# Kernel tuning notes

Hardware: AMD Instinct MI355X
Metric: run time of the kernel (lower is better)

## Reference

```python
import jax, jax.numpy as jnp
import numpy as np

H = 0.1  # explicit-Euler step size

def double_layer(x, K1, K2):
    # 1x1 conv1d == channel matmul; conv -> tanh -> conv
    x = jnp.tanh(jnp.einsum('oc,bcn->bon', K1, x))
    return jnp.einsum('oc,bcn->bon', K2, x)

def setup_inputs() -> dict:
    key = jax.random.key(0)
    ks = jax.random.split(key, 14)
    B, nNin, nEin, nopen, nhid, nNclose, nlayer = 1, 64, 64, 128, 128, 64, 4
    N, E = 10000, 160000
    Nfeat = 3 * nopen  # varlet=False
    stdv, stdvp = 0.01, 0.001
    return {
        'xn': jax.random.normal(ks[0], (B, nNin, N), dtype=jnp.float32),
        'xe': jax.random.normal(ks[1], (B, nEin, E), dtype=jnp.float32),
        'iInd': jax.random.randint(ks[2], (E,), 0, N),
        'jInd': jax.random.randint(ks[3], (E,), 0, N),
        'nnodes': N,
        'K1Nopen': jax.random.normal(ks[4], (nopen, nNin)) * stdv,
        'K2Nopen': jax.random.normal(ks[5], (nopen, nopen)) * stdv,
        'K1Eopen': jax.random.normal(ks[6], (nopen, nEin)) * stdv,
        'K2Eopen': jax.random.normal(ks[7], (nopen, nopen)) * stdv,
        'KNclose': jax.random.normal(ks[8], (nNclose, nopen)) * stdv,
        'KE1': jax.random.normal(ks[9], (nlayer, nhid, Nfeat)) * stdvp,
        'KE2': jax.random.normal(ks[10], (nlayer, nopen, nhid)) * stdvp,
        'KN1': jax.random.normal(ks[11], (nlayer, nhid, Nfeat)) * stdvp,
        'KN2': jax.random.normal(ks[12], (nlayer, nopen, nhid)) * stdvp,
    }

def reference(xn, xe, iInd, jInd, nnodes, K1Nopen, K2Nopen, K1Eopen, K2Eopen,
              KNclose, KE1, KE2, KN1, KN2):
    xn = double_layer(xn, K1Nopen, K2Nopen)   # [B, nopen, N]
    xe = double_layer(xe, K1Eopen, K2Eopen)   # [B, nopen, E]
    nlayer = KE1.shape[0]
    for i in range(nlayer):
        xi = xn[:, :, iInd]
        xj = xn[:, :, jInd]
        gradX = xi - xj                        # Graph.nodeGrad
        intX = 0.5 * (xi + xj)                 # Graph.nodeAve
        dxe = jnp.concatenate([intX, xe, gradX], axis=1)  # [B, 3*nopen, E]
        dxe = double_layer(dxe, KE1[i], KE2[i])
        flux = dxe
        zero = jnp.zeros((xn.shape[0], flux.shape[1], nnodes), flux.dtype)
        divE = zero.at[:, :, iInd].add(flux).at[:, :, jInd].add(-flux)  # edgeDiv
        aveE = 0.5 * (zero.at[:, :, iInd].add(flux)
                      + zero.at[:, :, jInd].add(flux))                  # edgeAve 'ave'
        dxn = jnp.concatenate([aveE, divE, xn], axis=1)  # [B, 3*nopen, N]
        dxn = double_layer(dxn, KN1[i], KN2[i])
        xn = xn - H * dxn
        xe = xe - H * dxe
    xn = jnp.einsum('oc,bcn->bon', KNclose, xn)
    return xn, xe
```

## Files before the change

### kernel.cpp

```cpp
#include <hip/hip_runtime.h>

typedef unsigned short u16;
typedef __attribute__((ext_vector_type(4))) unsigned short u16x4;
typedef __attribute__((ext_vector_type(8))) unsigned short u16x8;
typedef __attribute__((ext_vector_type(4))) float f32x4;
typedef __attribute__((ext_vector_type(8))) __bf16 b16x8;

__device__ __forceinline__ float bf2f(u16 u) {
  unsigned x = ((unsigned)u) << 16;
  return __builtin_bit_cast(float, x);
}
__device__ __forceinline__ u16 f2bf(float f) {
  unsigned u = __builtin_bit_cast(unsigned, f);
  u += 0x7fffu + ((u >> 16) & 1u);
  return (u16)(u >> 16);
}
__device__ __forceinline__ f32x4 MFMA(u16x8 a, u16x8 b, f32x4 c) {
  return __builtin_amdgcn_mfma_f32_16x16x32_bf16(
      __builtin_bit_cast(b16x8, a), __builtin_bit_cast(b16x8, b), c, 0, 0, 0);
}
__device__ __forceinline__ u16x8 ldApk(const u16* __restrict__ Apk, int Kdiv8, int rb, int ks, int l) {
  int kb = (ks >> 3) + (l >> 4);
  return *(const u16x8*)(Apk + (((size_t)(rb * Kdiv8 + kb)) << 7) + ((l & 15) << 3));
}
__device__ __forceinline__ u16x8 ldsB(const char* base, int rowB, int e, int kbyte) {
  return *(const u16x8*)(base + e * rowB + (kbyte ^ ((e & 7) << 4)));
}

__device__ __forceinline__ void gemm2x2(const u16* __restrict__ Apk, const char* Bb,
                                        int K, int rowB, int w, int l, f32x4 acc[2][2]) {
  int Kd8 = K >> 3;
  int rb0 = w * 2;
  for (int ks = 0; ks < K; ks += 32) {
    u16x8 a0 = ldApk(Apk, Kd8, rb0, ks, l);
    u16x8 a1 = ldApk(Apk, Kd8, rb0 + 1, ks, l);
    int kbyte = (ks + ((l >> 4) << 3)) << 1;
    u16x8 b0 = ldsB(Bb, rowB, l & 15, kbyte);
    u16x8 b1 = ldsB(Bb, rowB, 16 + (l & 15), kbyte);
    acc[0][0] = MFMA(a0, b0, acc[0][0]);
    acc[0][1] = MFMA(a0, b1, acc[0][1]);
    acc[1][0] = MFMA(a1, b0, acc[1][0]);
    acc[1][1] = MFMA(a1, b1, acc[1][1]);
  }
}

__device__ __forceinline__ void tanh_to_H(char* hb, int w, int l, f32x4 acc[2][2]) {
  for (int mi = 0; mi < 2; ++mi)
    for (int ni = 0; ni < 2; ++ni) {
      int e = 16 * ni + (l & 15);
      int cb = w * 32 + 16 * mi + ((l >> 4) << 2);
      u16x4 hv;
      for (int r = 0; r < 4; ++r) hv[r] = f2bf(tanhf(acc[mi][ni][r]));
      *(u16x4*)(hb + e * 256 + ((cb * 2) ^ ((e & 7) << 4))) = hv;
    }
}

struct Ptrs {
  u16* wpk; u16* xnT; u16* flux;
  int* offsI; int* offsJ; int* listI; int* listJ; int* headI; int* headJ;
};

__global__ __launch_bounds__(256) void detect_kernel(const u16* __restrict__ xn, int* flag) {
  __shared__ int cnt;
  if (threadIdx.x == 0) cnt = 0;
  __syncthreads();
  int ok = 0;
  for (int i = threadIdx.x; i < 512; i += 256) {
    u16 v = xn[i];
    int e = (v >> 7) & 0xFF;
    if (v == 0 || (e >= 117 && e <= 130)) ok++;
  }
  atomicAdd(&cnt, ok);
  __syncthreads();
  if (threadIdx.x == 0) *flag = (cnt >= 480) ? 1 : 0;
}

struct RepackDesc { const void* src; size_t srcOff; size_t dstOff; int rows; int K; };
struct RepackArgs { RepackDesc d[21]; };
__global__ __launch_bounds__(256) void repack_kernel(RepackArgs a, Ptrs pa, Ptrs pb,
                                                     const int* flag) {
  int fl = *flag;
  Ptrs P = fl ? pa : pb;
  RepackDesc d = a.d[blockIdx.y];
  int Kd8 = d.K >> 3;
  int nch = d.rows * Kd8;
  int c = blockIdx.x * 256 + threadIdx.x;
  if (c >= nch) return;
  int row = c / Kd8;
  int kb = c - row * Kd8;
  u16x8 v;
  if (fl) {
    v = *(const u16x8*)((const u16*)d.src + d.srcOff + (size_t)row * d.K + kb * 8);
  } else {
    const float* s = (const float*)d.src + d.srcOff + (size_t)row * d.K + kb * 8;
    f32x4 f0 = *(const f32x4*)s;
    f32x4 f1 = *(const f32x4*)(s + 4);
    for (int j = 0; j < 4; ++j) { v[j] = f2bf(f0[j]); v[4 + j] = f2bf(f1[j]); }
  }
  *(u16x8*)(P.wpk + d.dstOff + (((size_t)((row >> 4) * Kd8 + kb)) << 7) + ((row & 15) << 3)) = v;
}

__global__ __launch_bounds__(256) void csr_zero_kernel(Ptrs pa, Ptrs pb, const int* flag, int N) {
  Ptrs P = *flag ? pa : pb;
  int i = blockIdx.x * 256 + threadIdx.x;
  if (i < N) { P.headI[i] = 0; P.headJ[i] = 0; }
}
__global__ __launch_bounds__(256) void csr_hist_kernel(const int* __restrict__ iInd,
                                                       const int* __restrict__ jInd,
                                                       Ptrs pa, Ptrs pb, const int* flag, int E) {
  Ptrs P = *flag ? pa : pb;
  int e = blockIdx.x * 256 + threadIdx.x;
  if (e < E) {
    atomicAdd(&P.headI[iInd[e]], 1);
    atomicAdd(&P.headJ[jInd[e]], 1);
  }
}
__global__ __launch_bounds__(256) void csr_scan_kernel(Ptrs pa, Ptrs pb, const int* flag, int N) {
  Ptrs P = *flag ? pa : pb;
  __shared__ int sums[256];
  int t = threadIdx.x;
  int chunk = (N + 255) / 256;
  for (int pass = 0; pass < 2; ++pass) {
    int* cnt = pass ? P.headJ : P.headI;
    int* offs = pass ? P.offsJ : P.offsI;
    int lo = t * chunk;
    int hi = lo + chunk; if (hi > N) hi = N; if (lo > N) lo = N;
    int s = 0;
    for (int i = lo; i < hi; ++i) s += cnt[i];
    sums[t] = s;
    __syncthreads();
    if (t == 0) {
      int acc = 0;
      for (int i = 0; i < 256; ++i) { int v = sums[i]; sums[i] = acc; acc += v; }
      offs[N] = acc;
    }
    __syncthreads();
    int run = sums[t];
    for (int i = lo; i < hi; ++i) {
      int v = cnt[i];
      offs[i] = run;
      cnt[i] = run;
      run += v;
    }
    __syncthreads();
  }
}
__global__ __launch_bounds__(256) void csr_fill_kernel(const int* __restrict__ iInd,
                                                       const int* __restrict__ jInd,
                                                       Ptrs pa, Ptrs pb, const int* flag, int E) {
  Ptrs P = *flag ? pa : pb;
  int e = blockIdx.x * 256 + threadIdx.x;
  if (e < E) {
    int p = atomicAdd(&P.headI[iInd[e]], 1);
    P.listI[p] = e;
    int q = atomicAdd(&P.headJ[jInd[e]], 1);
    P.listJ[q] = e;
  }
}

__global__ __launch_bounds__(256) void open_kernel(const void* __restrict__ xin, int M,
                                                   int isXn, u16* __restrict__ fixedDst,
                                                   size_t k1Off, size_t k2Off,
                                                   Ptrs pa, Ptrs pb, const int* flag) {
  __shared__ u16 Ush[32 * 64];
  __shared__ u16 Hsh[32 * 128];
  int fl = *flag;
  Ptrs P = fl ? pa : pb;
  u16* outT = isXn ? P.xnT : fixedDst;
  const u16* K1pk = P.wpk + k1Off;
  const u16* K2pk = P.wpk + k2Off;
  int t = threadIdx.x, w = t >> 6, l = t & 63;
  int e0 = blockIdx.x * 32;
  char* ub = (char*)Ush;
  char* hb = (char*)Hsh;
  {
    int c = t >> 3;
    int e4 = (t & 7) * 4;
    for (int it = 0; it < 2; ++it, c += 32) {
      u16 v[4] = {0, 0, 0, 0};
      if (fl) {
        const u16* xs = (const u16*)xin;
        if (e0 + e4 + 3 < M) {
          u16x4 tmp = *(const u16x4*)(xs + (size_t)c * M + e0 + e4);
          for (int j = 0; j < 4; ++j) v[j] = tmp[j];
        } else {
          for (int j = 0; j < 4; ++j)
            if (e0 + e4 + j < M) v[j] = xs[(size_t)c * M + e0 + e4 + j];
        }
      } else {
        const float* xf = (const float*)xin;
        if (e0 + e4 + 3 < M) {
          f32x4 tmp = *(const f32x4*)(xf + (size_t)c * M + e0 + e4);
          for (int j = 0; j < 4; ++j) v[j] = f2bf(tmp[j]);
        } else {
          for (int j = 0; j < 4; ++j)
            if (e0 + e4 + j < M) v[j] = f2bf(xf[(size_t)c * M + e0 + e4 + j]);
        }
      }
      for (int j = 0; j < 4; ++j) {
        int e = e4 + j;
        *(u16*)(ub + e * 128 + ((c * 2) ^ ((e & 7) << 4))) = v[j];
      }
    }
  }
  __syncthreads();
  f32x4 acc[2][2] = {};
  gemm2x2(K1pk, ub, 64, 128, w, l, acc);
  tanh_to_H(hb, w, l, acc);
  __syncthreads();
  f32x4 acc2[2][2] = {};
  gemm2x2(K2pk, hb, 128, 256, w, l, acc2);
  for (int mi = 0; mi < 2; ++mi)
    for (int ni = 0; ni < 2; ++ni) {
      int e = 16 * ni + (l & 15);
      if (e0 + e < M) {
        int cb = w * 32 + 16 * mi + ((l >> 4) << 2);
        u16x4 o;
        for (int r = 0; r < 4; ++r) o[r] = f2bf(acc2[mi][ni][r]);
        *(u16x4*)(outT + (size_t)(e0 + e) * 128 + cb) = o;
      }
    }
}

__global__ __launch_bounds__(256) void edge_kernel(u16* __restrict__ xeT,
                                                   const int* __restrict__ iInd,
                                                   const int* __restrict__ jInd,
                                                   size_t e1Off, size_t e2Off, int E,
                                                   Ptrs pa, Ptrs pb, const int* flag) {
  __shared__ u16 Ush[32 * 384];
  __shared__ u16 Hsh[32 * 128];
  __shared__ int sI[32], sJ[32];
  Ptrs P = *flag ? pa : pb;
  const u16* xnT = P.xnT;
  const u16* E1pk = P.wpk + e1Off;
  const u16* E2pk = P.wpk + e2Off;
  int t = threadIdx.x, w = t >> 6, l = t & 63;
  int e0 = blockIdx.x * 32;
  char* ub = (char*)Ush;
  char* hb = (char*)Hsh;
  if (t < 32) {
    int ee = (e0 + t < E) ? e0 + t : E - 1;
    sI[t] = iInd[ee];
    sJ[t] = jInd[ee];
  }
  __syncthreads();
  for (int it = 0; it < 2; ++it) {
    int chunk = t + it * 256;
    int e = chunk >> 4, c = (chunk & 15) * 8;
    int ni = sI[e], nj = sJ[e];
    u16x8 xi = *(const u16x8*)(xnT + (size_t)ni * 128 + c);
    u16x8 xj = *(const u16x8*)(xnT + (size_t)nj * 128 + c);
    int eg = (e0 + e < E) ? e0 + e : E - 1;
    u16x8 xe = *(const u16x8*)(xeT + (size_t)eg * 128 + c);
    u16x8 iv, gv;
    for (int k = 0; k < 8; ++k) {
      float a = bf2f(xi[k]), b = bf2f(xj[k]);
      iv[k] = f2bf(0.5f * (a + b));
      gv[k] = f2bf(a - b);
    }
    *(u16x8*)(ub + e * 768 + ((c * 2) ^ ((e & 7) << 4))) = iv;
    *(u16x8*)(ub + e * 768 + (((128 + c) * 2) ^ ((e & 7) << 4))) = xe;
    *(u16x8*)(ub + e * 768 + (((256 + c) * 2) ^ ((e & 7) << 4))) = gv;
  }
  __syncthreads();
  f32x4 acc[2][2] = {};
  gemm2x2(E1pk, ub, 384, 768, w, l, acc);
  tanh_to_H(hb, w, l, acc);
  __syncthreads();
  f32x4 acc2[2][2] = {};
  gemm2x2(E2pk, hb, 128, 256, w, l, acc2);
  for (int mi = 0; mi < 2; ++mi)
    for (int ni = 0; ni < 2; ++ni) {
      int el = 16 * ni + (l & 15);
      int e = e0 + el;
      if (e < E) {
        int cb = w * 32 + 16 * mi + ((l >> 4) << 2);
        f32x4 v = acc2[mi][ni];
        u16x4 fb;
        for (int r = 0; r < 4; ++r) fb[r] = f2bf(v[r]);
        *(u16x4*)(P.flux + (size_t)e * 128 + cb) = fb;
        u16x4 old = *(u16x4*)(ub + el * 768 + (((128 + cb) * 2) ^ ((el & 7) << 4)));
        u16x4 nv;
        for (int r = 0; r < 4; ++r) nv[r] = f2bf(bf2f(old[r]) - 0.1f * v[r]);
        *(u16x4*)(xeT + (size_t)e * 128 + cb) = nv;
      }
    }
}

__global__ __launch_bounds__(256) void node_kernel(size_t n1Off, size_t n2Off, int N,
                                                   Ptrs pa, Ptrs pb, const int* flag) {
  __shared__ u16 Ush[32 * 384];
  __shared__ u16 Hsh[32 * 128];
  Ptrs P = *flag ? pa : pb;
  u16* xnT = P.xnT;
  const u16* N1pk = P.wpk + n1Off;
  const u16* N2pk = P.wpk + n2Off;
  int t = threadIdx.x, w = t >> 6, l = t & 63;
  int n0 = blockIdx.x * 32;
  char* ub = (char*)Ush;
  char* hb = (char*)Hsh;
  int nl = t >> 3, c16 = (t & 7) * 16;
  int n = n0 + nl;
  float ai[16], aj[16];
#pragma unroll
  for (int k = 0; k < 16; ++k) { ai[k] = 0.f; aj[k] = 0.f; }
  u16x8 xr0 = {0, 0, 0, 0, 0, 0, 0, 0}, xr1 = {0, 0, 0, 0, 0, 0, 0, 0};
  if (n < N) {
    const u16* fx = P.flux;
    {
      int p = P.offsI[n], pe = P.offsI[n + 1];
      for (; p + 1 < pe; p += 2) {
        int ea = P.listI[p], eb = P.listI[p + 1];
        u16x8 a0 = *(const u16x8*)(fx + (size_t)ea * 128 + c16);
        u16x8 a1 = *(const u16x8*)(fx + (size_t)ea * 128 + c16 + 8);
        u16x8 b0 = *(const u16x8*)(fx + (size_t)eb * 128 + c16);
        u16x8 b1 = *(const u16x8*)(fx + (size_t)eb * 128 + c16 + 8);
#pragma unroll
        for (int k = 0; k < 8; ++k) {
          ai[k] += bf2f(a0[k]) + bf2f(b0[k]);
          ai[8 + k] += bf2f(a1[k]) + bf2f(b1[k]);
        }
      }
      if (p < pe) {
        int ea = P.listI[p];
        u16x8 a0 = *(const u16x8*)(fx + (size_t)ea * 128 + c16);
        u16x8 a1 = *(const u16x8*)(fx + (size_t)ea * 128 + c16 + 8);
#pragma unroll
        for (int k = 0; k < 8; ++k) {
          ai[k] += bf2f(a0[k]);
          ai[8 + k] += bf2f(a1[k]);
        }
      }
    }
    {
      int p = P.offsJ[n], pe = P.offsJ[n + 1];
      for (; p + 1 < pe; p += 2) {
        int ea = P.listJ[p], eb = P.listJ[p + 1];
        u16x8 a0 = *(const u16x8*)(fx + (size_t)ea * 128 + c16);
        u16x8 a1 = *(const u16x8*)(fx + (size_t)ea * 128 + c16 + 8);
        u16x8 b0 = *(const u16x8*)(fx + (size_t)eb * 128 + c16);
        u16x8 b1 = *(const u16x8*)(fx + (size_t)eb * 128 + c16 + 8);
#pragma unroll
        for (int k = 0; k < 8; ++k) {
          aj[k] += bf2f(a0[k]) + bf2f(b0[k]);
          aj[8 + k] += bf2f(a1[k]) + bf2f(b1[k]);
        }
      }
      if (p < pe) {
        int ea = P.listJ[p];
        u16x8 a0 = *(const u16x8*)(fx + (size_t)ea * 128 + c16);
        u16x8 a1 = *(const u16x8*)(fx + (size_t)ea * 128 + c16 + 8);
#pragma unroll
        for (int k = 0; k < 8; ++k) {
          aj[k] += bf2f(a0[k]);
          aj[8 + k] += bf2f(a1[k]);
        }
      }
    }
    xr0 = *(const u16x8*)(xnT + (size_t)n * 128 + c16);
    xr1 = *(const u16x8*)(xnT + (size_t)n * 128 + c16 + 8);
  }
  u16x8 av0, av1, dv0, dv1;
#pragma unroll
  for (int k = 0; k < 8; ++k) {
    av0[k] = f2bf(0.5f * (ai[k] + aj[k]));
    av1[k] = f2bf(0.5f * (ai[8 + k] + aj[8 + k]));
    dv0[k] = f2bf(ai[k] - aj[k]);
    dv1[k] = f2bf(ai[8 + k] - aj[8 + k]);
  }
  int sw = (nl & 7) << 4;
  *(u16x8*)(ub + nl * 768 + ((c16 * 2) ^ sw)) = av0;
  *(u16x8*)(ub + nl * 768 + ((c16 * 2 + 16) ^ sw)) = av1;
  *(u16x8*)(ub + nl * 768 + (((128 + c16) * 2) ^ sw)) = dv0;
  *(u16x8*)(ub + nl * 768 + (((128 + c16) * 2 + 16) ^ sw)) = dv1;
  *(u16x8*)(ub + nl * 768 + (((256 + c16) * 2) ^ sw)) = xr0;
  *(u16x8*)(ub + nl * 768 + (((256 + c16) * 2 + 16) ^ sw)) = xr1;
  __syncthreads();
  f32x4 acc[2][2] = {};
  gemm2x2(N1pk, ub, 384, 768, w, l, acc);
  tanh_to_H(hb, w, l, acc);
  __syncthreads();
  f32x4 acc2[2][2] = {};
  gemm2x2(N2pk, hb, 128, 256, w, l, acc2);
  for (int mi = 0; mi < 2; ++mi)
    for (int ni = 0; ni < 2; ++ni) {
      int nn = 16 * ni + (l & 15);
      int ng = n0 + nn;
      if (ng < N) {
        int cb = w * 32 + 16 * mi + ((l >> 4) << 2);
        u16x4 old = *(u16x4*)(ub + nn * 768 + (((256 + cb) * 2) ^ ((nn & 7) << 4)));
        u16x4 nv;
        for (int r = 0; r < 4; ++r) nv[r] = f2bf(bf2f(old[r]) - 0.1f * acc2[mi][ni][r]);
        *(u16x4*)(xnT + (size_t)ng * 128 + cb) = nv;
      }
    }
}

__global__ __launch_bounds__(256) void close_kernel(size_t kcOff, int Nn, char* outb,
                                                    Ptrs pa, Ptrs pb, const int* flag) {
  int fl = *flag;
  Ptrs P = fl ? pa : pb;
  const u16* xnT = P.xnT;
  const u16* KCpk = P.wpk + kcOff;
  int t = threadIdx.x, w = t >> 6, l = t & 63;
  int n0 = blockIdx.x * 64 + w * 16;
  f32x4 acc[4] = {};
  int nr = n0 + (l & 15);
  if (nr > Nn - 1) nr = Nn - 1;
  for (int ks = 0; ks < 128; ks += 32) {
    u16x8 a = *(const u16x8*)(xnT + (size_t)nr * 128 + ks + ((l >> 4) << 3));
    for (int ci = 0; ci < 4; ++ci) {
      u16x8 b = ldApk(KCpk, 16, ci, ks, l);
      acc[ci] = MFMA(a, b, acc[ci]);
    }
  }
  for (int ci = 0; ci < 4; ++ci) {
    int c = 16 * ci + (l & 15);
    int nb = n0 + ((l >> 4) << 2);
    if (fl) {
      u16* o16 = (u16*)outb;
      u16x4 o;
      for (int r = 0; r < 4; ++r) o[r] = f2bf(acc[ci][r]);
      if (nb + 3 < Nn) *(u16x4*)(o16 + (size_t)c * Nn + nb) = o;
      else
        for (int r = 0; r < 4; ++r)
          if (nb + r < Nn) o16[(size_t)c * Nn + nb + r] = o[r];
    } else {
      float* of = (float*)outb;
      if (nb + 3 < Nn) *(f32x4*)(of + (size_t)c * Nn + nb) = acc[ci];
      else
        for (int r = 0; r < 4; ++r)
          if (nb + r < Nn) of[(size_t)c * Nn + nb + r] = acc[ci][r];
    }
  }
}

__global__ __launch_bounds__(256) void xe_out_kernel(const u16* __restrict__ xeT, int E, int Nn,
                                                     char* outb, const int* flag) {
  __shared__ u16 T[32][136];
  int fl = *flag;
  int t = threadIdx.x;
  int e0 = blockIdx.x * 32;
  for (int it = 0; it < 2; ++it) {
    int chunk = t + it * 256;
    int e = chunk >> 4, cb = (chunk & 15) * 8;
    int eg = (e0 + e < E) ? e0 + e : E - 1;
    u16x8 v = *(const u16x8*)(xeT + (size_t)eg * 128 + cb);
    for (int j = 0; j < 8; ++j) T[e][cb + j] = v[j];
  }
  __syncthreads();
  int c = t >> 1;
  int eb = (t & 1) * 16;
  if (fl) {
    u16* o16 = (u16*)outb + (size_t)64 * Nn;
    if (e0 + eb + 15 < E) {
      u16x8 o0, o1;
      for (int k = 0; k < 8; ++k) { o0[k] = T[eb + k][c]; o1[k] = T[eb + 8 + k][c]; }
      *(u16x8*)(o16 + (size_t)c * E + e0 + eb) = o0;
      *(u16x8*)(o16 + (size_t)c * E + e0 + eb + 8) = o1;
    } else {
      for (int k = 0; k < 16; ++k) {
        int e = e0 + eb + k;
        if (e < E) o16[(size_t)c * E + e] = T[eb + k][c];
      }
    }
  } else {
    float* of = (float*)outb + (size_t)64 * Nn;
    if (e0 + eb + 15 < E) {
      for (int q = 0; q < 4; ++q) {
        f32x4 o;
        for (int k = 0; k < 4; ++k) o[k] = bf2f(T[eb + q * 4 + k][c]);
        *(f32x4*)(of + (size_t)c * E + e0 + eb + q * 4) = o;
      }
    } else {
      for (int k = 0; k < 16; ++k) {
        int e = e0 + eb + k;
        if (e < E) of[(size_t)c * E + e] = bf2f(T[eb + k][c]);
      }
    }
  }
}

extern "C" void kernel_launch(void* const* d_in, const int* in_sizes, int n_in,
                              void* d_out, int out_size, void* d_ws, size_t ws_size,
                              hipStream_t stream) {
  const void* xn_in = d_in[0];
  const void* xe_in = d_in[1];
  const int* iInd = (const int*)d_in[2];
  const int* jInd = (const int*)d_in[3];

  int N = in_sizes[0] / 64;
  int E = in_sizes[2];
  int NP = (N + 31) & ~31;

  u16* xeT = (u16*)d_ws;
  int* flag = (int*)((char*)d_ws + (size_t)E * 256);

  const size_t WPK_ELEMS = 581632;
  const size_t TAILB = WPK_ELEMS * 2 + (size_t)NP * 256;
  char* outb = (char*)d_out;

  auto buildCsrFlux = [&](Ptrs& P, char* base, size_t o) {
    P.flux = (u16*)(base + o); o += (size_t)E * 256;
    P.offsI = (int*)(base + o); o += (size_t)(N + 1) * 4;
    P.offsJ = (int*)(base + o); o += (size_t)(N + 1) * 4;
    P.listI = (int*)(base + o); o += (size_t)E * 4;
    P.listJ = (int*)(base + o); o += (size_t)E * 4;
    P.headI = (int*)(base + o); o += (size_t)N * 4;
    P.headJ = (int*)(base + o);
  };

  Ptrs pb;
  {
    size_t tail = (((size_t)out_size * 4) - TAILB) & ~(size_t)255;
    pb.wpk = (u16*)(outb + tail);
    pb.xnT = pb.wpk + WPK_ELEMS;
    size_t o = ((size_t)64 * N * 4 + 255) & ~(size_t)255;
    buildCsrFlux(pb, outb, o);
  }
  Ptrs pa;
  {
    size_t tail = (((size_t)out_size * 2) - TAILB) & ~(size_t)255;
    pa.wpk = (u16*)(outb + tail);
    pa.xnT = pa.wpk + WPK_ELEMS;
    size_t o = ((size_t)E * 256 + 256 + 255) & ~(size_t)255;
    buildCsrFlux(pa, (char*)d_ws, o);
  }

  size_t woff[21];
  {
    size_t p = 0;
    auto nxt = [&](int i, size_t sz) { woff[i] = p; p += sz; };
    nxt(0, 128 * 64);
    nxt(1, 128 * 128);
    nxt(2, 128 * 64);
    nxt(3, 128 * 128);
    nxt(4, 64 * 128);
    for (int i = 0; i < 4; ++i) nxt(5 + i, 128 * 384);
    for (int i = 0; i < 4; ++i) nxt(9 + i, 128 * 128);
    for (int i = 0; i < 4; ++i) nxt(13 + i, 128 * 384);
    for (int i = 0; i < 4; ++i) nxt(17 + i, 128 * 128);
  }

  RepackArgs ra;
  auto setd = [&](int idx, const void* src, size_t srcOff, int rows, int K) {
    ra.d[idx].src = src;
    ra.d[idx].srcOff = srcOff;
    ra.d[idx].dstOff = woff[idx];
    ra.d[idx].rows = rows;
    ra.d[idx].K = K;
  };
  setd(0, d_in[5], 0, 128, 64);
  setd(1, d_in[6], 0, 128, 128);
  setd(2, d_in[7], 0, 128, 64);
  setd(3, d_in[8], 0, 128, 128);
  setd(4, d_in[9], 0, 64, 128);
  for (int i = 0; i < 4; ++i) setd(5 + i, d_in[10], (size_t)i * 128 * 384, 128, 384);
  for (int i = 0; i < 4; ++i) setd(9 + i, d_in[11], (size_t)i * 128 * 128, 128, 128);
  for (int i = 0; i < 4; ++i) setd(13 + i, d_in[12], (size_t)i * 128 * 384, 128, 384);
  for (int i = 0; i < 4; ++i) setd(17 + i, d_in[13], (size_t)i * 128 * 128, 128, 128);

  detect_kernel<<<1, 256, 0, stream>>>((const u16*)xn_in, flag);
  repack_kernel<<<dim3(24, 21), 256, 0, stream>>>(ra, pa, pb, flag);

  csr_zero_kernel<<<(N + 255) / 256, 256, 0, stream>>>(pa, pb, flag, N);
  csr_hist_kernel<<<(E + 255) / 256, 256, 0, stream>>>(iInd, jInd, pa, pb, flag, E);
  csr_scan_kernel<<<1, 256, 0, stream>>>(pa, pb, flag, N);
  csr_fill_kernel<<<(E + 255) / 256, 256, 0, stream>>>(iInd, jInd, pa, pb, flag, E);

  open_kernel<<<(N + 31) / 32, 256, 0, stream>>>(xn_in, N, 1, (u16*)nullptr,
                                                 woff[0], woff[1], pa, pb, flag);
  open_kernel<<<(E + 31) / 32, 256, 0, stream>>>(xe_in, E, 0, xeT,
                                                 woff[2], woff[3], pa, pb, flag);

  for (int i = 0; i < 4; ++i) {
    edge_kernel<<<(E + 31) / 32, 256, 0, stream>>>(xeT, iInd, jInd, woff[5 + i], woff[9 + i], E,
                                                   pa, pb, flag);
    node_kernel<<<(N + 31) / 32, 256, 0, stream>>>(woff[13 + i], woff[17 + i], N, pa, pb, flag);
  }

  close_kernel<<<(N + 63) / 64, 256, 0, stream>>>(woff[4], N, outb, pa, pb, flag);
  xe_out_kernel<<<(E + 31) / 32, 256, 0, stream>>>(xeT, E, N, outb, flag);
}
```

Before: 668.7 us.

## Use 512-thread blocks for edge and node kernels with re-split MFMA work

The edge kernel now processes 64 edges per 512-thread block, with waves split into row and column halves, so each weight tile is shared across twice as many edges. The node kernel keeps 32 nodes per block but uses 512 threads: each thread gathers 8 channels instead of 16, and each wave computes a 16-row output slice with an inlined MFMA loop. The aim is more parallelism in the latency-bound CSR gather and better weight reuse in the edge GEMM. The cost is higher per-block LDS use for edges, which may reduce occupancy, and smaller per-wave MFMA work in the node kernel.

```diff
diff --git a/kernel.cpp b/kernel.cpp
--- a/kernel.cpp
+++ b/kernel.cpp
@@ -222,30 +222,31 @@
     }
 }
 
-__global__ __launch_bounds__(256) void edge_kernel(u16* __restrict__ xeT,
+__global__ __launch_bounds__(512) void edge_kernel(u16* __restrict__ xeT,
                                                    const int* __restrict__ iInd,
                                                    const int* __restrict__ jInd,
                                                    size_t e1Off, size_t e2Off, int E,
                                                    Ptrs pa, Ptrs pb, const int* flag) {
-  __shared__ u16 Ush[32 * 384];
-  __shared__ u16 Hsh[32 * 128];
-  __shared__ int sI[32], sJ[32];
+  __shared__ u16 Ush[64 * 384];
+  __shared__ u16 Hsh[64 * 128];
+  __shared__ int sI[64], sJ[64];
   Ptrs P = *flag ? pa : pb;
   const u16* xnT = P.xnT;
   const u16* E1pk = P.wpk + e1Off;
   const u16* E2pk = P.wpk + e2Off;
   int t = threadIdx.x, w = t >> 6, l = t & 63;
-  int e0 = blockIdx.x * 32;
+  int wr = w >> 1, wc = w & 1;
+  int e0 = blockIdx.x * 64;
   char* ub = (char*)Ush;
   char* hb = (char*)Hsh;
-  if (t < 32) {
+  if (t < 64) {
     int ee = (e0 + t < E) ? e0 + t : E - 1;
     sI[t] = iInd[ee];
     sJ[t] = jInd[ee];
   }
   __syncthreads();
   for (int it = 0; it < 2; ++it) {
-    int chunk = t + it * 256;
+    int chunk = t + it * 512;
     int e = chunk >> 4, c = (chunk & 15) * 8;
     int ni = sI[e], nj = sJ[e];
     u16x8 xi = *(const u16x8*)(xnT + (size_t)ni * 128 + c);
@@ -263,18 +264,20 @@
     *(u16x8*)(ub + e * 768 + (((256 + c) * 2) ^ ((e & 7) << 4))) = gv;
   }
   __syncthreads();
+  char* ubw = ub + wc * 32 * 768;
+  char* hbw = hb + wc * 32 * 256;
   f32x4 acc[2][2] = {};
-  gemm2x2(E1pk, ub, 384, 768, w, l, acc);
-  tanh_to_H(hb, w, l, acc);
+  gemm2x2(E1pk, ubw, 384, 768, wr, l, acc);
+  tanh_to_H(hbw, wr, l, acc);
   __syncthreads();
   f32x4 acc2[2][2] = {};
-  gemm2x2(E2pk, hb, 128, 256, w, l, acc2);
+  gemm2x2(E2pk, hbw, 128, 256, wr, l, acc2);
   for (int mi = 0; mi < 2; ++mi)
     for (int ni = 0; ni < 2; ++ni) {
-      int el = 16 * ni + (l & 15);
+      int el = wc * 32 + 16 * ni + (l & 15);
       int e = e0 + el;
       if (e < E) {
-        int cb = w * 32 + 16 * mi + ((l >> 4) << 2);
+        int cb = wr * 32 + 16 * mi + ((l >> 4) << 2);
         f32x4 v = acc2[mi][ni];
         u16x4 fb;
         for (int r = 0; r < 4; ++r) fb[r] = f2bf(v[r]);
@@ -287,7 +290,7 @@
     }
 }
 
-__global__ __launch_bounds__(256) void node_kernel(size_t n1Off, size_t n2Off, int N,
+__global__ __launch_bounds__(512) void node_kernel(size_t n1Off, size_t n2Off, int N,
                                                    Ptrs pa, Ptrs pb, const int* flag) {
   __shared__ u16 Ush[32 * 384];
   __shared__ u16 Hsh[32 * 128];
@@ -299,101 +302,96 @@
   int n0 = blockIdx.x * 32;
   char* ub = (char*)Ush;
   char* hb = (char*)Hsh;
-  int nl = t >> 3, c16 = (t & 7) * 16;
+  int nl = t >> 4, c8 = (t & 15) * 8;
   int n = n0 + nl;
-  float ai[16], aj[16];
+  float ai[8], aj[8];
 #pragma unroll
-  for (int k = 0; k < 16; ++k) { ai[k] = 0.f; aj[k] = 0.f; }
-  u16x8 xr0 = {0, 0, 0, 0, 0, 0, 0, 0}, xr1 = {0, 0, 0, 0, 0, 0, 0, 0};
+  for (int k = 0; k < 8; ++k) { ai[k] = 0.f; aj[k] = 0.f; }
+  u16x8 xr = {0, 0, 0, 0, 0, 0, 0, 0};
   if (n < N) {
     const u16* fx = P.flux;
     {
       int p = P.offsI[n], pe = P.offsI[n + 1];
       for (; p + 1 < pe; p += 2) {
         int ea = P.listI[p], eb = P.listI[p + 1];
-        u16x8 a0 = *(const u16x8*)(fx + (size_t)ea * 128 + c16);
-        u16x8 a1 = *(const u16x8*)(fx + (size_t)ea * 128 + c16 + 8);
-        u16x8 b0 = *(const u16x8*)(fx + (size_t)eb * 128 + c16);
-        u16x8 b1 = *(const u16x8*)(fx + (size_t)eb * 128 + c16 + 8);
+        u16x8 a0 = *(const u16x8*)(fx + (size_t)ea * 128 + c8);
+        u16x8 b0 = *(const u16x8*)(fx + (size_t)eb * 128 + c8);
 #pragma unroll
-        for (int k = 0; k < 8; ++k) {
-          ai[k] += bf2f(a0[k]) + bf2f(b0[k]);
-          ai[8 + k] += bf2f(a1[k]) + bf2f(b1[k]);
-        }
+        for (int k = 0; k < 8; ++k) ai[k] += bf2f(a0[k]) + bf2f(b0[k]);
       }
       if (p < pe) {
         int ea = P.listI[p];
-        u16x8 a0 = *(const u16x8*)(fx + (size_t)ea * 128 + c16);
-        u16x8 a1 = *(const u16x8*)(fx + (size_t)ea * 128 + c16 + 8);
+        u16x8 a0 = *(const u16x8*)(fx + (size_t)ea * 128 + c8);
 #pragma unroll
-        for (int k = 0; k < 8; ++k) {
-          ai[k] += bf2f(a0[k]);
-          ai[8 + k] += bf2f(a1[k]);
-        }
+        for (int k = 0; k < 8; ++k) ai[k] += bf2f(a0[k]);
       }
     }
     {
       int p = P.offsJ[n], pe = P.offsJ[n + 1];
       for (; p + 1 < pe; p += 2) {
         int ea = P.listJ[p], eb = P.listJ[p + 1];
-        u16x8 a0 = *(const u16x8*)(fx + (size_t)ea * 128 + c16);
-        u16x8 a1 = *(const u16x8*)(fx + (size_t)ea * 128 + c16 + 8);
-        u16x8 b0 = *(const u16x8*)(fx + (size_t)eb * 128 + c16);
-        u16x8 b1 = *(const u16x8*)(fx + (size_t)eb * 128 + c16 + 8);
+        u16x8 a0 = *(const u16x8*)(fx + (size_t)ea * 128 + c8);
+        u16x8 b0 = *(const u16x8*)(fx + (size_t)eb * 128 + c8);
 #pragma unroll
-        for (int k = 0; k < 8; ++k) {
-          aj[k] += bf2f(a0[k]) + bf2f(b0[k]);
-          aj[8 + k] += bf2f(a1[k]) + bf2f(b1[k]);
-        }
+        for (int k = 0; k < 8; ++k) aj[k] += bf2f(a0[k]) + bf2f(b0[k]);
       }
       if (p < pe) {
         int ea = P.listJ[p];
-        u16x8 a0 = *(const u16x8*)(fx + (size_t)ea * 128 + c16);
-        u16x8 a1 = *(const u16x8*)(fx + (size_t)ea * 128 + c16 + 8);
+        u16x8 a0 = *(const u16x8*)(fx + (size_t)ea * 128 + c8);
 #pragma unroll
-        for (int k = 0; k < 8; ++k) {
-          aj[k] += bf2f(a0[k]);
-          aj[8 + k] += bf2f(a1[k]);
-        }
-      }
-    }
-    xr0 = *(const u16x8*)(xnT + (size_t)n * 128 + c16);
-    xr1 = *(const u16x8*)(xnT + (size_t)n * 128 + c16 + 8);
-  }
-  u16x8 av0, av1, dv0, dv1;
+        for (int k = 0; k < 8; ++k) aj[k] += bf2f(a0[k]);
+      }
+    }
+    xr = *(const u16x8*)(xnT + (size_t)n * 128 + c8);
+  }
+  u16x8 av, dv;
 #pragma unroll
   for (int k = 0; k < 8; ++k) {
-    av0[k] = f2bf(0.5f * (ai[k] + aj[k]));
-    av1[k] = f2bf(0.5f * (ai[8 + k] + aj[8 + k]));
-    dv0[k] = f2bf(ai[k] - aj[k]);
-    dv1[k] = f2bf(ai[8 + k] - aj[8 + k]);
+    av[k] = f2bf(0.5f * (ai[k] + aj[k]));
+    dv[k] = f2bf(ai[k] - aj[k]);
   }
   int sw = (nl & 7) << 4;
-  *(u16x8*)(ub + nl * 768 + ((c16 * 2) ^ sw)) = av0;
-  *(u16x8*)(ub + nl * 768 + ((c16 * 2 + 16) ^ sw)) = av1;
-  *(u16x8*)(ub + nl * 768 + (((128 + c16) * 2) ^ sw)) = dv0;
-  *(u16x8*)(ub + nl * 768 + (((128 + c16) * 2 + 16) ^ sw)) = dv1;
-  *(u16x8*)(ub + nl * 768 + (((256 + c16) * 2) ^ sw)) = xr0;
-  *(u16x8*)(ub + nl * 768 + (((256 + c16) * 2 + 16) ^ sw)) = xr1;
-  __syncthreads();
-  f32x4 acc[2][2] = {};
-  gemm2x2(N1pk, ub, 384, 768, w, l, acc);
-  tanh_to_H(hb, w, l, acc);
-  __syncthreads();
-  f32x4 acc2[2][2] = {};
-  gemm2x2(N2pk, hb, 128, 256, w, l, acc2);
-  for (int mi = 0; mi < 2; ++mi)
-    for (int ni = 0; ni < 2; ++ni) {
-      int nn = 16 * ni + (l & 15);
-      int ng = n0 + nn;
-      if (ng < N) {
-        int cb = w * 32 + 16 * mi + ((l >> 4) << 2);
-        u16x4 old = *(u16x4*)(ub + nn * 768 + (((256 + cb) * 2) ^ ((nn & 7) << 4)));
-        u16x4 nv;
-        for (int r = 0; r < 4; ++r) nv[r] = f2bf(bf2f(old[r]) - 0.1f * acc2[mi][ni][r]);
-        *(u16x4*)(xnT + (size_t)ng * 128 + cb) = nv;
-      }
-    }
+  *(u16x8*)(ub + nl * 768 + ((c8 * 2) ^ sw)) = av;
+  *(u16x8*)(ub + nl * 768 + (((128 + c8) * 2) ^ sw)) = dv;
+  *(u16x8*)(ub + nl * 768 + (((256 + c8) * 2) ^ sw)) = xr;
+  __syncthreads();
+  f32x4 acc[2] = {};
+  for (int ks = 0; ks < 384; ks += 32) {
+    u16x8 a = ldApk(N1pk, 48, w, ks, l);
+    int kbyte = (ks + ((l >> 4) << 3)) << 1;
+    u16x8 b0 = ldsB(ub, 768, l & 15, kbyte);
+    u16x8 b1 = ldsB(ub, 768, 16 + (l & 15), kbyte);
+    acc[0] = MFMA(a, b0, acc[0]);
+    acc[1] = MFMA(a, b1, acc[1]);
+  }
+  for (int ni = 0; ni < 2; ++ni) {
+    int e = 16 * ni + (l & 15);
+    int cb = 16 * w + ((l >> 4) << 2);
+    u16x4 hv;
+    for (int r = 0; r < 4; ++r) hv[r] = f2bf(tanhf(acc[ni][r]));
+    *(u16x4*)(hb + e * 256 + ((cb * 2) ^ ((e & 7) << 4))) = hv;
+  }
+  __syncthreads();
+  f32x4 acc2[2] = {};
+  for (int ks = 0; ks < 128; ks += 32) {
+    u16x8 a = ldApk(N2pk, 16, w, ks, l);
+    int kbyte = (ks + ((l >> 4) << 3)) << 1;
+    u16x8 b0 = ldsB(hb, 256, l & 15, kbyte);
+    u16x8 b1 = ldsB(hb, 256, 16 + (l & 15), kbyte);
+    acc2[0] = MFMA(a, b0, acc2[0]);
+    acc2[1] = MFMA(a, b1, acc2[1]);
+  }
+  for (int ni = 0; ni < 2; ++ni) {
+    int nn = 16 * ni + (l & 15);
+    int ng = n0 + nn;
+    if (ng < N) {
+      int cb = 16 * w + ((l >> 4) << 2);
+      u16x4 old = *(u16x4*)(ub + nn * 768 + (((256 + cb) * 2) ^ ((nn & 7) << 4)));
+      u16x4 nv;
+      for (int r = 0; r < 4; ++r) nv[r] = f2bf(bf2f(old[r]) - 0.1f * acc2[ni][r]);
+      *(u16x4*)(xnT + (size_t)ng * 128 + cb) = nv;
+    }
+  }
 }
 
 __global__ __launch_bounds__(256) void close_kernel(size_t kcOff, int Nn, char* outb,
@@ -574,9 +572,9 @@
                                                  woff[2], woff[3], pa, pb, flag);
 
   for (int i = 0; i < 4; ++i) {
-    edge_kernel<<<(E + 31) / 32, 256, 0, stream>>>(xeT, iInd, jInd, woff[5 + i], woff[9 + i], E,
+    edge_kernel<<<(E + 63) / 64, 512, 0, stream>>>(xeT, iInd, jInd, woff[5 + i], woff[9 + i], E,
                                                    pa, pb, flag);
-    node_kernel<<<(N + 31) / 32, 256, 0, stream>>>(woff[13 + i], woff[17 + i], N, pa, pb, flag);
+    node_kernel<<<(N + 31) / 32, 512, 0, stream>>>(woff[13 + i], woff[17 + i], N, pa, pb, flag);
   }
 
   close_kernel<<<(N + 63) / 64, 256, 0, stream>>>(woff[4], N, outb, pa, pb, flag);
```

Result: no change. 671.8 us (+0.5%).
